# Kernel optimization log

Measured on AMD Instinct MI355X. Metric: run time of the kernel, lower is better.

Reference implementation:

```python
import jax, jax.numpy as jnp
import numpy as np

TOPK = 2
DN = ('NCHW', 'OIHW', 'NCHW')

def gelu(x):
    return jax.nn.gelu(x, approximate=False)

def conv2d(x, w, b, stride, padding, groups):
    y = jax.lax.conv_general_dilated(x, w, stride, padding,
                                     dimension_numbers=DN, feature_group_count=groups)
    return y if b is None else y + b[None, :, None, None]

def setup_inputs() -> dict:
    key = jax.random.key(0)
    ks = jax.random.split(key, 24)
    C, E, L, B, H, W = 64, 4, 5, 16, 160, 160  # L = max low_dim = num_experts+1 (linear growth i+2)
    s = 0.05
    rn = lambda k, shp: jax.random.normal(k, shp, jnp.float32) * s
    d = {}
    d['x'] = jax.random.normal(ks[0], (B, C, H, W), jnp.float32)
    d['c1_w1'] = rn(ks[1], (C, C, 3, 3)); d['c1_b1'] = rn(ks[2], (C,))
    d['c1_w2'] = rn(ks[3], (2 * C, C, 1, 1)); d['c1_b2'] = rn(ks[4], (2 * C,))
    d['agg_w'] = rn(ks[5], (C, 1, 4, 4)); d['agg_b'] = rn(ks[6], (C,))
    d['cal_dw_w'] = rn(ks[7], (C, 1, 3, 3)); d['cal_dw_b'] = rn(ks[8], (C,))
    d['cal_pw_w'] = rn(ks[9], (C, C, 1, 1)); d['cal_pw_b'] = rn(ks[10], (C,))
    d['sc_w1'] = rn(ks[11], (C, 1, 1, 3)); d['sc_b1'] = rn(ks[12], (C,))
    d['sc_w2'] = rn(ks[13], (C, 1, 3, 1)); d['sc_b2'] = rn(ks[14], (C,))
    d['gate_w'] = rn(ks[15], (E, C))
    # Experts have varying low_dim (i+2); zero-pad to L so they stack. Padded
    # channels are exactly zero through the conv1*conv2 product, so math matches.
    rng = np.random.default_rng(0)
    ew1 = np.zeros((E, L, C), np.float32); eb1 = np.zeros((E, L), np.float32)
    ew2 = np.zeros((E, L, C), np.float32); eb2 = np.zeros((E, L), np.float32)
    ew3 = np.zeros((E, C, L), np.float32); eb3 = np.zeros((E, C), np.float32)
    for i in range(E):
        low = i + 2
        ew1[i, :low] = rng.normal(size=(low, C)) * s; eb1[i, :low] = rng.normal(size=(low,)) * s
        ew2[i, :low] = rng.normal(size=(low, C)) * s; eb2[i, :low] = rng.normal(size=(low,)) * s
        ew3[i, :, :low] = rng.normal(size=(C, low)) * s; eb3[i] = rng.normal(size=(C,)) * s
    d['e_w1'] = jnp.asarray(ew1); d['e_b1'] = jnp.asarray(eb1)
    d['e_w2'] = jnp.asarray(ew2); d['e_b2'] = jnp.asarray(eb2)
    d['e_w3'] = jnp.asarray(ew3); d['e_b3'] = jnp.asarray(eb3)
    d['proj_w'] = rn(ks[16], (C, C, 1, 1)); d['proj_b'] = rn(ks[17], (C,))
    return d

def reference(x, c1_w1, c1_b1, c1_w2, c1_b2, agg_w, agg_b, cal_dw_w, cal_dw_b,
              cal_pw_w, cal_pw_b, sc_w1, sc_b1, sc_w2, sc_b2, gate_w,
              e_w1, e_b1, e_w2, e_b2, e_w3, e_b3, proj_w, proj_b):
    B, C = x.shape[0], x.shape[1]
    P1 = [(1, 1), (1, 1)]; P0 = [(0, 0), (0, 0)]
    # conv_1: 3x3 -> GELU -> 1x1 (C -> 2C)
    h = gelu(conv2d(x, c1_w1, c1_b1, (1, 1), P1, 1))
    h = conv2d(h, c1_w2, c1_b2, (1, 1), P0, 1)
    # channel shuffle, groups=2
    b_, c2, hh, ww = h.shape
    h = h.reshape(b_, 2, c2 // 2, hh, ww).transpose(0, 2, 1, 3, 4).reshape(b_, c2, hh, ww)
    xs, k = h[:, :C], h[:, C:]
    # conv_2: striped depthwise (1,3) then (3,1), then GELU
    xs = conv2d(xs, sc_w1, sc_b1, (1, 1), [(0, 0), (1, 1)], C)
    xs = gelu(conv2d(xs, sc_w2, sc_b2, (1, 1), [(1, 1), (0, 0)], C))
    # calibrate(k): recursive depthwise stride-4 downsample, conv, bilinear upsample, residual
    res = k
    for _ in range(2):
        k = gelu(conv2d(k, agg_w, agg_b, (4, 4), [(2, 2), (2, 2)], C))
    k = conv2d(k, cal_dw_w, cal_dw_b, (1, 1), P1, C)
    k = conv2d(k, cal_pw_w, cal_pw_b, (1, 1), P0, 1)
    k = res + jax.image.resize(k, res.shape, method='bilinear')
    # router: global avg pool -> linear (no bias) -> softmax (fp32)
    logits = jnp.mean(xs, axis=(2, 3)) @ gate_w.T  # [B, E]
    weights = jax.nn.softmax(logits.astype(jnp.float32), axis=1).astype(xs.dtype)
    vals, idx = jax.lax.top_k(weights, TOPK)
    exp_w = jnp.zeros_like(weights).at[jnp.arange(B)[:, None], idx].set(vals)  # masked top-k weights
    # dense experts (training path): out = xs + sum_e w_be * Expert_e(xs, k)
    a = jnp.einsum('elc,bchw->belhw', e_w1, xs) + e_b1[None, :, :, None, None]
    bb = jnp.einsum('elc,bchw->belhw', e_w2, k) + e_b2[None, :, :, None, None]
    p = a * bb  # [B, E, L, H, W]
    out = xs + jnp.einsum('be,ecl,belhw->bchw', exp_w, e_w3, p) \
             + jnp.einsum('be,ec->bc', exp_w, e_b3)[:, :, None, None]
    return conv2d(out, proj_w, proj_b, (1, 1), P0, 1)
```

## Files before the change

### kernel.cpp

```cpp
#include <hip/hip_runtime.h>
#include <hip/hip_bf16.h>
#include <math.h>
#include <stdint.h>

typedef __hip_bfloat16 bf16;

__device__ __forceinline__ float b2f(bf16 v){ return __bfloat162float(v); }
__device__ __forceinline__ bf16  f2b(float v){ return __float2bfloat16(v); }
__device__ __forceinline__ float gelu_f(float x){ return 0.5f*x*(1.0f+erff(x*0.70710678118654752f)); }
__device__ __forceinline__ float tof(float v){ return v; }
__device__ __forceinline__ float tof(bf16 v){ return __bfloat162float(v); }

#define SC8  16.0f
#define ISC8 0.0625f
__device__ __forceinline__ uint8_t f2e4(float v){
  int r = __builtin_amdgcn_cvt_pk_fp8_f32(v*SC8, v*SC8, 0, false);
  return (uint8_t)(r & 0xFF);
}
__device__ __forceinline__ float e42f(uint8_t b){
  return __builtin_amdgcn_cvt_f32_fp8((int)b, 0) * ISC8;
}

typedef __bf16 bf16x8 __attribute__((ext_vector_type(8)));
typedef float  f32x4  __attribute__((ext_vector_type(4)));
typedef short  v8s    __attribute__((ext_vector_type(8)));
union Frag { bf16x8 v; unsigned short u[8]; };

__device__ __forceinline__ unsigned short bfb(float v){
  union { bf16 h; unsigned short u; } cv; cv.h = f2b(v); return cv.u;
}
__device__ __forceinline__ float bfu2f(unsigned short u){
  union { float f; unsigned u32; } x; x.u32 = ((unsigned)u) << 16; return x.f;
}
__device__ __forceinline__ bf16x8 ldsb8(const short* p){
  return *reinterpret_cast<const bf16x8*>(p);
}
__device__ __forceinline__ int SW8(int w){ return ((w ^ (w >> 3)) & 7) << 3; }


__global__ __launch_bounds__(256) void k_tr(const float* __restrict__ x,
                                            bf16* __restrict__ xT){
  __shared__ __align__(16) short LT[160*64];
  int bid = blockIdx.x;
  int h = bid % 160;
  int b = bid / 160;
  int tid = threadIdx.x;
  #pragma unroll
  for (int i=0;i<5;i++){
    int q = tid + i*256;
    int ci0 = (q/40)*2;
    int w4  = (q - (q/40)*40)*4;
    const float* pa = x + (((b*64 + ci0)*160 + h)*160) + w4;
    float4 fa = *reinterpret_cast<const float4*>(pa);
    float4 fb = *reinterpret_cast<const float4*>(pa + 25600);
    float va[4] = {fa.x, fa.y, fa.z, fa.w};
    float vb[4] = {fb.x, fb.y, fb.z, fb.w};
    #pragma unroll
    for (int j=0;j<4;j++){
      int w = w4 + j;
      unsigned pk = (unsigned)bfb(va[j]) | ((unsigned)bfb(vb[j]) << 16);
      int slot = w*64 + (ci0 ^ SW8(w));
      *reinterpret_cast<unsigned*>(&LT[slot]) = pk;
    }
  }
  __syncthreads();
  bf16* dst = xT + ((size_t)(b*160 + h))*160*64;
  #pragma unroll
  for (int i=0;i<5;i++){
    int k = tid + i*256;
    int w = k >> 3;
    int ci0 = (k & 7) << 3;
    v8s v = *reinterpret_cast<const v8s*>(&LT[w*64 + (ci0 ^ SW8(w))]);
    *reinterpret_cast<v8s*>(dst + w*64 + ci0) = v;
  }
}

__global__ __launch_bounds__(256) void k_conv12(const bf16* __restrict__ xT,
                                                const float* __restrict__ w1,
                                                const float* __restrict__ b1,
                                                const float* __restrict__ w2,
                                                const float* __restrict__ b2,
                                                bf16* __restrict__ xs0,
                                                bf16* __restrict__ k0){
  __shared__ __align__(16) short Xs[16128];
  __shared__ __align__(16) short H1[5120];
  int bid = blockIdx.x;
  int half = bid & 1;
  int bh = bid >> 1;
  int h = bh % 160;
  int b = bh / 160;
  int w0 = half*80;
  int tid = threadIdx.x;
  int lane = tid & 63;
  int wv = tid >> 6;
  int c = lane & 15;
  int g = lane >> 4;

  Frag wf[18];
  {
    int co = wv*16 + c;
    const float* wbase = w1 + co*576 + g*72;
    #pragma unroll
    for (int r=0;r<3;r++){
      #pragma unroll
      for (int s=0;s<3;s++){
        #pragma unroll
        for (int kk=0;kk<2;kk++){
          Frag f;
          #pragma unroll
          for (int e=0;e<8;e++)
            f.u[e] = bfb(wbase[kk*288 + e*9 + r*3 + s]);
          wf[(r*3+s)*2+kk] = f;
        }
      }
    }
  }

  {
    const bf16* xTb = xT + (size_t)b*160*160*64;
    #pragma unroll
    for (int it=0; it<8; ++it){
      int q = tid + it*256;
      if (q < 2016){
        int r   = q / 672;
        int rem = q - r*672;
        int col = rem >> 3;
        int ci0 = (rem & 7) << 3;
        int gh  = h - 1 + r;
        int gw  = w0 - 1 + col;
        v8s val = {0,0,0,0,0,0,0,0};
        if ((unsigned)gh < 160u && (unsigned)gw < 160u)
          val = *reinterpret_cast<const v8s*>(xTb + (gh*160 + gw)*64 + ci0);
        int eidx = (r*84 + col)*64 + (ci0 ^ ((col & 7) << 3));
        *reinterpret_cast<v8s*>(&Xs[eidx]) = val;
      }
    }
  }
  __syncthreads();

  float bb1r[4];
  {
    const float* bp = b1 + wv*16 + g*4;
    #pragma unroll
    for (int r=0;r<4;r++) bb1r[r] = bp[r];
  }
  int bB[3][2];
  #pragma unroll
  for (int s=0;s<3;s++){
    #pragma unroll
    for (int kk=0;kk<2;kk++)
      bB[s][kk] = (c + s)*64 + ((kk*32 + g*8) ^ (((c + s) & 7) << 3));
  }
  #pragma unroll 1
  for (int n=0;n<5;++n){
    f32x4 acc0 = {0.f,0.f,0.f,0.f};
    f32x4 acc1 = {0.f,0.f,0.f,0.f};
    #pragma unroll
    for (int r=0;r<3;r++){
      #pragma unroll
      for (int s=0;s<3;s++){
        int base = r*5376 + n*1024;
        bf16x8 bf0 = ldsb8(&Xs[bB[s][0] + base]);
        bf16x8 bf1 = ldsb8(&Xs[bB[s][1] + base]);
        int t = (r*3 + s)*2;
        acc0 = __builtin_amdgcn_mfma_f32_16x16x32_bf16(wf[t].v,   bf0, acc0, 0, 0, 0);
        acc1 = __builtin_amdgcn_mfma_f32_16x16x32_bf16(wf[t+1].v, bf1, acc1, 0, 0, 0);
      }
    }
    unsigned long long pk = 0ull;
    #pragma unroll
    for (int r=0;r<4;r++){
      float v = gelu_f(acc0[r] + acc1[r] + bb1r[r]);
      pk |= ((unsigned long long)bfb(v)) << (16*r);
    }
    int eH = (n*16 + c)*64 + ((wv*16 + g*4) ^ ((c & 7) << 3));
    *reinterpret_cast<unsigned long long*>(&H1[eH]) = pk;
  }
  __syncthreads();

  Frag w2f[4];
  {
    #pragma unroll
    for (int j=0;j<2;j++){
      #pragma unroll
      for (int kk=0;kk<2;kk++){
        const float* wp = w2 + (wv*32 + j*16 + c)*64 + kk*32 + g*8;
        Frag f;
        #pragma unroll
        for (int e=0;e<8;e++) f.u[e] = bfb(wp[e]);
        w2f[j*2+kk] = f;
      }
    }
  }
  float bb2r[2][4];
  #pragma unroll
  for (int j=0;j<2;j++){
    const float* bp = b2 + wv*32 + j*16 + g*4;
    #pragma unroll
    for (int r=0;r<4;r++) bb2r[j][r] = bp[r];
  }
  int posb = h*160 + w0 + c;
  int sb[2][4]; int flg[2][4];
  #pragma unroll
  for (int j=0;j<2;j++){
    #pragma unroll
    for (int r=0;r<4;r++){
      int o = wv*32 + j*16 + g*4 + r;
      int n2 = ((o & 63) << 1) | (o >> 6);
      if (n2 < 64){ sb[j][r] = (b*64 + n2)*25600 + posb;        flg[j][r] = 1; }
      else        { sb[j][r] = (b*64 + (n2-64))*25600 + posb;   flg[j][r] = 0; }
    }
  }
  int bH0 = c*64 + ((g*8)      ^ ((c & 7) << 3));
  int bH1 = c*64 + ((32 + g*8) ^ ((c & 7) << 3));
  #pragma unroll 1
  for (int n=0;n<5;++n){
    bf16x8 h0 = ldsb8(&H1[bH0 + n*1024]);
    bf16x8 h1 = ldsb8(&H1[bH1 + n*1024]);
    #pragma unroll
    for (int j=0;j<2;j++){
      f32x4 acc = {0.f,0.f,0.f,0.f};
      acc = __builtin_amdgcn_mfma_f32_16x16x32_bf16(w2f[j*2].v,   h0, acc, 0, 0, 0);
      acc = __builtin_amdgcn_mfma_f32_16x16x32_bf16(w2f[j*2+1].v, h1, acc, 0, 0, 0);
      #pragma unroll
      for (int r=0;r<4;r++){
        float v = acc[r] + bb2r[j][r];
        bf16 bv = f2b(v);
        if (flg[j][r]) xs0[sb[j][r] + n*16] = bv;
        else           k0 [sb[j][r] + n*16] = bv;
      }
    }
  }
}

__global__ __launch_bounds__(256) void k_sc(const bf16* __restrict__ xs0,
                                            const float* __restrict__ scw1,
                                            const float* __restrict__ scb1,
                                            const float* __restrict__ scw2,
                                            const float* __restrict__ scb2,
                                            bf16* __restrict__ xsf){
  int t = blockIdx.x*256 + threadIdx.x;
  int w8 = (t % 20) * 8;
  int r2 = t / 20;
  int h  = r2 % 160;
  int bc = r2 / 160;
  int c  = bc & 63;
  const bf16* plane = xs0 + (size_t)bc*25600;
  float w1a = scw1[c*3], w1b = scw1[c*3+1], w1c = scw1[c*3+2];
  float b1  = scb1[c];
  float w2a = scw2[c*3], w2b = scw2[c*3+1], w2c = scw2[c*3+2];
  float b2v = scb2[c];
  float acc[8];
  #pragma unroll
  for (int j=0;j<8;j++) acc[j] = b2v;
  #pragma unroll
  for (int dh=0; dh<3; dh++){
    int hh = h-1+dh;
    if ((unsigned)hh < 160u){
      const bf16* row = plane + hh*160;
      float wnd[10];
      v8s mv = *reinterpret_cast<const v8s*>(row + w8);
      #pragma unroll
      for (int j=0;j<8;j++) wnd[j+1] = bfu2f((unsigned short)mv[j]);
      wnd[0] = (w8 > 0)   ? b2f(row[w8-1]) : 0.f;
      wnd[9] = (w8 < 152) ? b2f(row[w8+8]) : 0.f;
      float w2h = (dh==0)?w2a:((dh==1)?w2b:w2c);
      #pragma unroll
      for (int j=0;j<8;j++){
        float inner = fmaf(w1a, wnd[j], fmaf(w1b, wnd[j+1], fmaf(w1c, wnd[j+2], b1)));
        acc[j] = fmaf(w2h, inner, acc[j]);
      }
    }
  }
  v8s o;
  #pragma unroll
  for (int j=0;j<8;j++) o[j] = (short)bfb(gelu_f(acc[j]));
  *reinterpret_cast<v8s*>(xsf + (size_t)bc*25600 + h*160 + w8) = o;
}

__global__ __launch_bounds__(256) void k_mean(const bf16* __restrict__ xsf, float* __restrict__ meanX){
  int bc = blockIdx.x;
  const bf16* p = xsf + (size_t)bc*25600;
  float s = 0.f;
  for (int i = threadIdx.x; i < 3200; i += 256){
    v8s v = *reinterpret_cast<const v8s*>(p + i*8);
    #pragma unroll
    for (int j=0;j<8;j++) s += bfu2f((unsigned short)v[j]);
  }
  __shared__ float red[256];
  red[threadIdx.x] = s; __syncthreads();
  for (int st=128; st>0; st>>=1){
    if (threadIdx.x < st) red[threadIdx.x] += red[threadIdx.x+st];
    __syncthreads();
  }
  if (threadIdx.x==0) meanX[bc] = red[0]*(1.0f/25600.0f);
}

template<typename Tin>
__global__ __launch_bounds__(256) void k_agg(const Tin* __restrict__ in,
                                             const float* __restrict__ aggw,
                                             const float* __restrict__ aggb,
                                             float* __restrict__ out,
                                             int IH, int OH, int total){
  int t = blockIdx.x*256+threadIdx.x;
  if (t >= total) return;
  int ow = t % OH;
  int oh = (t/OH) % OH;
  int c  = (t/(OH*OH)) & 63;
  int bc = t/(OH*OH);
  const Tin* ip = in + (size_t)bc*IH*IH;
  const float* Wp = aggw + c*16;
  float acc = aggb[c];
  #pragma unroll
  for (int kh=0;kh<4;kh++){
    int ih = oh*4 - 2 + kh;
    if ((unsigned)ih < (unsigned)IH){
      #pragma unroll
      for (int kw=0;kw<4;kw++){
        int iw = ow*4 - 2 + kw;
        if ((unsigned)iw < (unsigned)IH)
          acc = fmaf(Wp[kh*4+kw], tof(ip[ih*IH+iw]), acc);
      }
    }
  }
  out[t] = gelu_f(acc);
}

__global__ __launch_bounds__(256) void k_caldw(const float* __restrict__ A2,
                                               const float* __restrict__ dww,
                                               const float* __restrict__ dwb,
                                               float* __restrict__ T1){
  int t = blockIdx.x*256+threadIdx.x;
  if (t >= 16*64*121) return;
  int pw = t % 11;
  int ph = (t/11) % 11;
  int c  = (t/121) & 63;
  int bc = t/121;
  const float* ip = A2 + bc*121;
  const float* Wp = dww + c*9;
  float acc = dwb[c];
  #pragma unroll
  for (int kh=0;kh<3;kh++){
    int ih = ph-1+kh;
    if ((unsigned)ih < 11u){
      #pragma unroll
      for (int kw=0;kw<3;kw++){
        int iw = pw-1+kw;
        if ((unsigned)iw < 11u)
          acc = fmaf(Wp[kh*3+kw], ip[ih*11+iw], acc);
      }
    }
  }
  T1[t] = acc;
}

__global__ __launch_bounds__(256) void k_calpw(const float* __restrict__ T1,
                                               const float* __restrict__ pww,
                                               const float* __restrict__ pwb,
                                               float* __restrict__ KSo){
  int t = blockIdx.x*256+threadIdx.x;
  if (t >= 16*64*121) return;
  int p  = t % 121;
  int co = (t/121) & 63;
  int b  = t/(121*64);
  const float* Wp = pww + co*64;
  const float* ip = T1 + b*64*121 + p;
  float acc = pwb[co];
  for (int ci=0;ci<64;ci++) acc = fmaf(Wp[ci], ip[ci*121], acc);
  KSo[t] = acc;
}

__global__ __launch_bounds__(64) void k_gate(const float* __restrict__ meanX,
                                             const float* __restrict__ gatew,
                                             float* __restrict__ expw){
  __shared__ float lg[64];
  int t = threadIdx.x;
  int b = t>>2, e = t&3;
  const float* g = gatew + e*64;
  const float* m = meanX + b*64;
  float s = 0.f;
  for (int c2=0;c2<64;c2++) s += g[c2]*m[c2];
  lg[t] = s;
  __syncthreads();
  if (e==0){
    float v0=lg[t], v1=lg[t+1], v2=lg[t+2], v3=lg[t+3];
    float mx = fmaxf(fmaxf(v0,v1), fmaxf(v2,v3));
    float p[4];
    p[0]=expf(v0-mx); p[1]=expf(v1-mx); p[2]=expf(v2-mx); p[3]=expf(v3-mx);
    float sum = p[0]+p[1]+p[2]+p[3];
    float inv = 1.0f/sum;
    p[0]*=inv; p[1]*=inv; p[2]*=inv; p[3]*=inv;
    int i1 = 0;
    for (int i=1;i<4;i++) if (p[i] > p[i1]) i1 = i;
    int i2 = -1;
    for (int i=0;i<4;i++){ if (i==i1) continue; if (i2<0 || p[i]>p[i2]) i2 = i; }
    for (int i=0;i<4;i++) expw[b*4+i] = (i==i1||i==i2)? p[i] : 0.f;
  }
}

__global__ __launch_bounds__(256) void k_pw3(const float* __restrict__ ew3,
                                             const float* __restrict__ eb3,
                                             const float* __restrict__ projw,
                                             float* __restrict__ pw3,
                                             float* __restrict__ pb3){
  int t = blockIdx.x*256+threadIdx.x;
  if (t >= 64*24) return;
  int r = t/24, q = t%24;
  const float* P = projw + r*64;
  if (q < 20){
    int e=q/5, l=q%5;
    float s=0.f;
    for (int c=0;c<64;c++) s = fmaf(P[c], ew3[(e*64+c)*5 + l], s);
    pw3[r*20+q] = s;
  } else {
    int e = q-20;
    float s=0.f;
    for (int c=0;c<64;c++) s = fmaf(P[c], eb3[e*64 + c], s);
    pb3[r*4+e] = s;
  }
}

__global__ __launch_bounds__(256) void k_kk(const bf16* __restrict__ k0,
                                            const float* __restrict__ KSi,
                                            uint8_t* __restrict__ kk8){
  int tt = blockIdx.x*256 + threadIdx.x;
  int bc = tt / 3200;
  int rr = tt - bc*3200;
  int ph = rr / 20;
  int pw0 = (rr - ph*20) * 8;
  float shf = (ph+0.5f)*0.06875f - 0.5f;
  int ihf = (int)floorf(shf); float th = shf - (float)ihf;
  int i0 = min(max(ihf,0),10), i1 = min(max(ihf+1,0),10);
  const float* ksp = KSi + bc*121;
  size_t base = (size_t)bc*25600 + ph*160 + pw0;
  v8s kv = *reinterpret_cast<const v8s*>(k0 + base);
  unsigned long long o = 0ull;
  #pragma unroll
  for (int j=0;j<8;j++){
    int pw = pw0 + j;
    float swf = (pw+0.5f)*0.06875f - 0.5f;
    int iwf = (int)floorf(swf); float tw = swf - (float)iwf;
    int j0 = min(max(iwf,0),10), j1 = min(max(iwf+1,0),10);
    float v00 = ksp[i0*11+j0], v01 = ksp[i0*11+j1];
    float v10 = ksp[i1*11+j0], v11 = ksp[i1*11+j1];
    float vtop = v00 + tw*(v01-v00);
    float vbot = v10 + tw*(v11-v10);
    float val = bfu2f((unsigned short)kv[j]) + (vtop + th*(vbot-vtop));
    o |= ((unsigned long long)f2e4(val)) << (8*j);
  }
  *reinterpret_cast<unsigned long long*>(kk8 + base) = o;
}

__global__ __launch_bounds__(256) void k_final(const bf16* __restrict__ xsf,
                                               const uint8_t* __restrict__ kk8,
                                               const float* __restrict__ expw,
                                               const float* __restrict__ pw3,
                                               const float* __restrict__ pb3,
                                               const float* __restrict__ ew1,
                                               const float* __restrict__ eb1,
                                               const float* __restrict__ ew2,
                                               const float* __restrict__ eb2,
                                               const float* __restrict__ projw,
                                               const float* __restrict__ projb,
                                               float* __restrict__ out){
  __shared__ float XS[4096];
  __shared__ float KK[4096];
  __shared__ float PP[1280];
  int bid = blockIdx.x;
  int pt = bid % 400;
  int b  = bid / 400;
  int p0 = pt<<6;
  int tid = threadIdx.x;
  int lane = tid & 63;
  for (int cw = tid; cw < 512; cw += 256){
    int c = cw >> 3, w0 = (cw & 7) << 3;
    size_t gi = (size_t)(b*64+c)*25600 + p0 + w0;
    v8s xv = *reinterpret_cast<const v8s*>(xsf + gi);
    unsigned long long kv = *reinterpret_cast<const unsigned long long*>(kk8 + gi);
    #pragma unroll
    for (int j=0;j<8;j++){
      XS[(c<<6)+w0+j] = bfu2f((unsigned short)xv[j]);
      KK[(c<<6)+w0+j] = e42f((uint8_t)((kv >> (8*j)) & 0xFF));
    }
  }
  __syncthreads();
  int wv = __builtin_amdgcn_readfirstlane(tid>>6);
  {
    int e = wv;
    float a[5], bb[5];
    #pragma unroll
    for (int l=0;l<5;l++) a[l] = eb1[e*5 + l];
    const float* W1 = ew1 + e*5*64;
    for (int c=0;c<64;c++){
      float xv = XS[(c<<6)+lane];
      #pragma unroll
      for (int l=0;l<5;l++) a[l] = fmaf(W1[l*64+c], xv, a[l]);
    }
    #pragma unroll
    for (int l=0;l<5;l++) bb[l] = eb2[e*5 + l];
    const float* W2 = ew2 + e*5*64;
    for (int c=0;c<64;c++){
      float kv = KK[(c<<6)+lane];
      #pragma unroll
      for (int l=0;l<5;l++) bb[l] = fmaf(W2[l*64+c], kv, bb[l]);
    }
    float we = expw[b*4 + e];
    #pragma unroll
    for (int l=0;l<5;l++) PP[(e*5+l)*64 + lane] = we * a[l]*bb[l];
  }
  __syncthreads();
  float ew0 = expw[b*4+0], ewa = expw[b*4+1], ewb = expw[b*4+2], ewc = expw[b*4+3];
  for (int qg=0; qg<4; qg++){
    int r0 = (wv<<4) + (qg<<2);
    float y[4];
    #pragma unroll
    for (int q=0;q<4;q++){
      int r = r0+q;
      y[q] = projb[r] + ew0*pb3[r*4+0] + ewa*pb3[r*4+1] + ewb*pb3[r*4+2] + ewc*pb3[r*4+3];
    }
    const float* Pw = projw + r0*64;
    for (int c=0;c<64;c++){
      float xv = XS[(c<<6)+lane];
      y[0]=fmaf(Pw[c]     ,xv,y[0]);
      y[1]=fmaf(Pw[64+c]  ,xv,y[1]);
      y[2]=fmaf(Pw[128+c] ,xv,y[2]);
      y[3]=fmaf(Pw[192+c] ,xv,y[3]);
    }
    const float* Qw = pw3 + r0*20;
    for (int j=0;j<20;j++){
      float pv = PP[(j<<6)+lane];
      y[0]=fmaf(Qw[j]    ,pv,y[0]);
      y[1]=fmaf(Qw[20+j] ,pv,y[1]);
      y[2]=fmaf(Qw[40+j] ,pv,y[2]);
      y[3]=fmaf(Qw[60+j] ,pv,y[3]);
    }
    #pragma unroll
    for (int q=0;q<4;q++)
      out[(size_t)(b*64+r0+q)*25600 + p0 + lane] = y[q];
  }
}

static constexpr size_t OB_XT   = 0;
static constexpr size_t OB_K0   = 52428800;
static constexpr size_t OB_MEAN = 0;
static constexpr size_t OB_KS   = 65536;
static constexpr size_t OB_A2   = 1048576;
static constexpr size_t OB_T1   = 2097152;
static constexpr size_t OB_A1   = 4194304;
static constexpr size_t XB_XS0  = 0;
static constexpr size_t XB_KK8  = 0;
static constexpr size_t XB_EXPW = 26214400;
static constexpr size_t XB_PW3  = 26218496;
static constexpr size_t XB_PB3  = 26226688;
static constexpr size_t XB_XSF  = 52428800;

extern "C" void kernel_launch(void* const* d_in, const int* in_sizes, int n_in,
                              void* d_out, int out_size, void* d_ws, size_t ws_size,
                              hipStream_t stream){
  (void)in_sizes; (void)n_in; (void)out_size; (void)d_ws; (void)ws_size;
  const float* x     = (const float*)d_in[0];
  char* xb           = (char*)d_in[0];
  const float* c1w1  = (const float*)d_in[1];
  const float* c1b1  = (const float*)d_in[2];
  const float* c1w2  = (const float*)d_in[3];
  const float* c1b2  = (const float*)d_in[4];
  const float* aggw  = (const float*)d_in[5];
  const float* aggb  = (const float*)d_in[6];
  const float* dww   = (const float*)d_in[7];
  const float* dwb   = (const float*)d_in[8];
  const float* pww   = (const float*)d_in[9];
  const float* pwb   = (const float*)d_in[10];
  const float* scw1  = (const float*)d_in[11];
  const float* scb1  = (const float*)d_in[12];
  const float* scw2  = (const float*)d_in[13];
  const float* scb2  = (const float*)d_in[14];
  const float* gatew = (const float*)d_in[15];
  const float* ew1   = (const float*)d_in[16];
  const float* eb1   = (const float*)d_in[17];
  const float* ew2   = (const float*)d_in[18];
  const float* eb2   = (const float*)d_in[19];
  const float* ew3   = (const float*)d_in[20];
  const float* eb3   = (const float*)d_in[21];
  const float* projw = (const float*)d_in[22];
  const float* projb = (const float*)d_in[23];

  char* ob = (char*)d_out;
  bf16* xT     = (bf16*)(ob + OB_XT);
  bf16* k0     = (bf16*)(ob + OB_K0);
  float* meanX = (float*)(ob + OB_MEAN);
  float* KS    = (float*)(ob + OB_KS);
  float* A2    = (float*)(ob + OB_A2);
  float* T1    = (float*)(ob + OB_T1);
  float* A1    = (float*)(ob + OB_A1);
  bf16* xs0    = (bf16*)(xb + XB_XS0);
  uint8_t* kk8 = (uint8_t*)(xb + XB_KK8);
  float* expw  = (float*)(xb + XB_EXPW);
  float* pw3   = (float*)(xb + XB_PW3);
  float* pb3   = (float*)(xb + XB_PB3);
  bf16* xsf    = (bf16*)(xb + XB_XSF);
  float* outp  = (float*)d_out;

  k_tr     <<<2560,     256, 0, stream>>>(x, xT);
  k_conv12 <<<5120,     256, 0, stream>>>(xT, c1w1, c1b1, c1w2, c1b2, xs0, k0);
  k_sc     <<<12800,    256, 0, stream>>>(xs0, scw1, scb1, scw2, scb2, xsf);
  k_mean   <<<1024,     256, 0, stream>>>(xsf, meanX);
  k_agg<bf16> <<<6724,  256, 0, stream>>>(k0, aggw, aggb, A1, 160, 41, 16*64*41*41);
  k_agg<float><<<484,   256, 0, stream>>>(A1, aggw, aggb, A2, 41, 11, 16*64*11*11);
  k_caldw  <<<484,      256, 0, stream>>>(A2, dww, dwb, T1);
  k_calpw  <<<484,      256, 0, stream>>>(T1, pww, pwb, KS);
  k_gate   <<<1,         64, 0, stream>>>(meanX, gatew, expw);
  k_pw3    <<<6,        256, 0, stream>>>(ew3, eb3, projw, pw3, pb3);
  k_kk     <<<12800,    256, 0, stream>>>(k0, KS, kk8);
  k_final  <<<16*400,   256, 0, stream>>>(xsf, kk8, expw, pw3, pb3,
                                          ew1, eb1, ew2, eb2, projw, projb, outp);
}
```

Baseline: 621.6 us.

## Fuse mean into shortcut kernel and fuse aggregation chain into one kernel

The global-average-pool mean is now computed inside the shortcut-conv kernel with a wavefront shuffle reduction and atomicAdd, after zeroing the buffer in a small kernel. This removes the separate full re-read of xsf. The two stride-4 aggregation convs and the depthwise calibration conv are fused into one kernel per (b,c) plane that stages the plane in LDS and keeps the intermediates in shared memory, which removes the global A1/A2 round-trips and two launches. In exchange, atomics make the summation order nondeterministic. The large LDS footprint of about 58KB per block limits occupancy of the fused kernel to 1024 blocks.

```diff
diff --git a/kernel.cpp b/kernel.cpp
--- a/kernel.cpp
+++ b/kernel.cpp
@@ -8,8 +8,6 @@
 __device__ __forceinline__ float b2f(bf16 v){ return __bfloat162float(v); }
 __device__ __forceinline__ bf16  f2b(float v){ return __float2bfloat16(v); }
 __device__ __forceinline__ float gelu_f(float x){ return 0.5f*x*(1.0f+erff(x*0.70710678118654752f)); }
-__device__ __forceinline__ float tof(float v){ return v; }
-__device__ __forceinline__ float tof(bf16 v){ return __bfloat162float(v); }
 
 #define SC8  16.0f
 #define ISC8 0.0625f
@@ -73,6 +71,10 @@
     v8s v = *reinterpret_cast<const v8s*>(&LT[w*64 + (ci0 ^ SW8(w))]);
     *reinterpret_cast<v8s*>(dst + w*64 + ci0) = v;
   }
+}
+
+__global__ __launch_bounds__(256) void k_zero(float* __restrict__ p){
+  p[blockIdx.x*256 + threadIdx.x] = 0.f;
 }
 
 __global__ __launch_bounds__(256) void k_conv12(const bf16* __restrict__ xT,
@@ -238,7 +240,8 @@
                                             const float* __restrict__ scb1,
                                             const float* __restrict__ scw2,
                                             const float* __restrict__ scb2,
-                                            bf16* __restrict__ xsf){
+                                            bf16* __restrict__ xsf,
+                                            float* __restrict__ meanX){
   int t = blockIdx.x*256 + threadIdx.x;
   int w8 = (t % 20) * 8;
   int r2 = t / 20;
@@ -273,85 +276,92 @@
     }
   }
   v8s o;
-  #pragma unroll
-  for (int j=0;j<8;j++) o[j] = (short)bfb(gelu_f(acc[j]));
+  float ls = 0.f;
+  #pragma unroll
+  for (int j=0;j<8;j++){
+    unsigned short ub = bfb(gelu_f(acc[j]));
+    o[j] = (short)ub;
+    ls += bfu2f(ub);
+  }
   *reinterpret_cast<v8s*>(xsf + (size_t)bc*25600 + h*160 + w8) = o;
-}
-
-__global__ __launch_bounds__(256) void k_mean(const bf16* __restrict__ xsf, float* __restrict__ meanX){
+  #pragma unroll
+  for (int off=32; off>0; off>>=1) ls += __shfl_down(ls, off);
+  if ((threadIdx.x & 63) == 0) atomicAdd(&meanX[bc], ls*(1.0f/25600.0f));
+}
+
+__global__ __launch_bounds__(256) void k_aggfuse(const bf16* __restrict__ k0,
+                                                 const float* __restrict__ aggw,
+                                                 const float* __restrict__ aggb,
+                                                 const float* __restrict__ dww,
+                                                 const float* __restrict__ dwb,
+                                                 float* __restrict__ T1){
+  __shared__ __align__(16) short KP[25600];
+  __shared__ float A1L[1681];
+  __shared__ float A2L[121];
   int bc = blockIdx.x;
-  const bf16* p = xsf + (size_t)bc*25600;
-  float s = 0.f;
-  for (int i = threadIdx.x; i < 3200; i += 256){
-    v8s v = *reinterpret_cast<const v8s*>(p + i*8);
-    #pragma unroll
-    for (int j=0;j<8;j++) s += bfu2f((unsigned short)v[j]);
-  }
-  __shared__ float red[256];
-  red[threadIdx.x] = s; __syncthreads();
-  for (int st=128; st>0; st>>=1){
-    if (threadIdx.x < st) red[threadIdx.x] += red[threadIdx.x+st];
-    __syncthreads();
-  }
-  if (threadIdx.x==0) meanX[bc] = red[0]*(1.0f/25600.0f);
-}
-
-template<typename Tin>
-__global__ __launch_bounds__(256) void k_agg(const Tin* __restrict__ in,
-                                             const float* __restrict__ aggw,
-                                             const float* __restrict__ aggb,
-                                             float* __restrict__ out,
-                                             int IH, int OH, int total){
-  int t = blockIdx.x*256+threadIdx.x;
-  if (t >= total) return;
-  int ow = t % OH;
-  int oh = (t/OH) % OH;
-  int c  = (t/(OH*OH)) & 63;
-  int bc = t/(OH*OH);
-  const Tin* ip = in + (size_t)bc*IH*IH;
-  const float* Wp = aggw + c*16;
-  float acc = aggb[c];
-  #pragma unroll
-  for (int kh=0;kh<4;kh++){
-    int ih = oh*4 - 2 + kh;
-    if ((unsigned)ih < (unsigned)IH){
-      #pragma unroll
-      for (int kw=0;kw<4;kw++){
-        int iw = ow*4 - 2 + kw;
-        if ((unsigned)iw < (unsigned)IH)
-          acc = fmaf(Wp[kh*4+kw], tof(ip[ih*IH+iw]), acc);
-      }
-    }
-  }
-  out[t] = gelu_f(acc);
-}
-
-__global__ __launch_bounds__(256) void k_caldw(const float* __restrict__ A2,
-                                               const float* __restrict__ dww,
-                                               const float* __restrict__ dwb,
-                                               float* __restrict__ T1){
-  int t = blockIdx.x*256+threadIdx.x;
-  if (t >= 16*64*121) return;
-  int pw = t % 11;
-  int ph = (t/11) % 11;
-  int c  = (t/121) & 63;
-  int bc = t/121;
-  const float* ip = A2 + bc*121;
-  const float* Wp = dww + c*9;
-  float acc = dwb[c];
-  #pragma unroll
-  for (int kh=0;kh<3;kh++){
-    int ih = ph-1+kh;
-    if ((unsigned)ih < 11u){
-      #pragma unroll
-      for (int kw=0;kw<3;kw++){
-        int iw = pw-1+kw;
-        if ((unsigned)iw < 11u)
-          acc = fmaf(Wp[kh*3+kw], ip[ih*11+iw], acc);
-      }
-    }
-  }
-  T1[t] = acc;
+  int c = bc & 63;
+  int tid = threadIdx.x;
+  const bf16* src = k0 + (size_t)bc*25600;
+  for (int i=tid; i<3200; i+=256)
+    *reinterpret_cast<v8s*>(&KP[i*8]) = *reinterpret_cast<const v8s*>(src + i*8);
+  float wgt[16];
+  #pragma unroll
+  for (int q=0;q<16;q++) wgt[q] = aggw[c*16+q];
+  float bia = aggb[c];
+  __syncthreads();
+  for (int i=tid; i<1681; i+=256){
+    int oh = i/41, ow = i - oh*41;
+    float acc = bia;
+    #pragma unroll
+    for (int kh=0;kh<4;kh++){
+      int ih = oh*4-2+kh;
+      if ((unsigned)ih < 160u){
+        #pragma unroll
+        for (int kw=0;kw<4;kw++){
+          int iw = ow*4-2+kw;
+          if ((unsigned)iw < 160u)
+            acc = fmaf(wgt[kh*4+kw], bfu2f((unsigned short)KP[ih*160+iw]), acc);
+        }
+      }
+    }
+    A1L[i] = gelu_f(acc);
+  }
+  __syncthreads();
+  if (tid < 121){
+    int ph = tid/11, pw = tid - ph*11;
+    float acc = bia;
+    #pragma unroll
+    for (int kh=0;kh<4;kh++){
+      int ih = ph*4-2+kh;
+      if ((unsigned)ih < 41u){
+        #pragma unroll
+        for (int kw=0;kw<4;kw++){
+          int iw = pw*4-2+kw;
+          if ((unsigned)iw < 41u)
+            acc = fmaf(wgt[kh*4+kw], A1L[ih*41+iw], acc);
+        }
+      }
+    }
+    A2L[tid] = gelu_f(acc);
+  }
+  __syncthreads();
+  if (tid < 121){
+    int ph = tid/11, pw = tid - ph*11;
+    float acc = dwb[c];
+    #pragma unroll
+    for (int kh=0;kh<3;kh++){
+      int ih = ph-1+kh;
+      if ((unsigned)ih < 11u){
+        #pragma unroll
+        for (int kw=0;kw<3;kw++){
+          int iw = pw-1+kw;
+          if ((unsigned)iw < 11u)
+            acc = fmaf(dww[c*9+kh*3+kw], A2L[ih*11+iw], acc);
+        }
+      }
+    }
+    T1[(size_t)bc*121 + tid] = acc;
+  }
 }
 
 __global__ __launch_bounds__(256) void k_calpw(const float* __restrict__ T1,
@@ -544,9 +554,7 @@
 static constexpr size_t OB_K0   = 52428800;
 static constexpr size_t OB_MEAN = 0;
 static constexpr size_t OB_KS   = 65536;
-static constexpr size_t OB_A2   = 1048576;
 static constexpr size_t OB_T1   = 2097152;
-static constexpr size_t OB_A1   = 4194304;
 static constexpr size_t XB_XS0  = 0;
 static constexpr size_t XB_KK8  = 0;
 static constexpr size_t XB_EXPW = 26214400;
@@ -589,9 +597,7 @@
   bf16* k0     = (bf16*)(ob + OB_K0);
   float* meanX = (float*)(ob + OB_MEAN);
   float* KS    = (float*)(ob + OB_KS);
-  float* A2    = (float*)(ob + OB_A2);
   float* T1    = (float*)(ob + OB_T1);
-  float* A1    = (float*)(ob + OB_A1);
   bf16* xs0    = (bf16*)(xb + XB_XS0);
   uint8_t* kk8 = (uint8_t*)(xb + XB_KK8);
   float* expw  = (float*)(xb + XB_EXPW);
@@ -602,11 +608,9 @@
 
   k_tr     <<<2560,     256, 0, stream>>>(x, xT);
   k_conv12 <<<5120,     256, 0, stream>>>(xT, c1w1, c1b1, c1w2, c1b2, xs0, k0);
-  k_sc     <<<12800,    256, 0, stream>>>(xs0, scw1, scb1, scw2, scb2, xsf);
-  k_mean   <<<1024,     256, 0, stream>>>(xsf, meanX);
-  k_agg<bf16> <<<6724,  256, 0, stream>>>(k0, aggw, aggb, A1, 160, 41, 16*64*41*41);
-  k_agg<float><<<484,   256, 0, stream>>>(A1, aggw, aggb, A2, 41, 11, 16*64*11*11);
-  k_caldw  <<<484,      256, 0, stream>>>(A2, dww, dwb, T1);
+  k_zero   <<<4,        256, 0, stream>>>(meanX);
+  k_sc     <<<12800,    256, 0, stream>>>(xs0, scw1, scb1, scw2, scb2, xsf, meanX);
+  k_aggfuse<<<1024,     256, 0, stream>>>(k0, aggw, aggb, dww, dwb, T1);
   k_calpw  <<<484,      256, 0, stream>>>(T1, pww, pwb, KS);
   k_gate   <<<1,         64, 0, stream>>>(meanX, gatew, expw);
   k_pw3    <<<6,        256, 0, stream>>>(ew3, eb3, projw, pw3, pb3);
```

Result: slower. 647.2 us (+4.1%).

## Process 5-row strips in conv12 with rolling halo buffer; fuse mean into sc

Applied to the files above, without the earlier changes.

Each conv12 block now handles a strip of 5 output rows instead of one row. It keeps a 4-slot ring buffer of input rows in LDS and prefetches the next row into registers while the current row's MFMAs run. This cuts the 3x halo reload of input rows and amortizes the per-block weight fragment loads over more rows. Separately, the global-mean kernel is removed: k_sc accumulates per-wavefront partial sums into meanX with atomics after a small zeroing kernel. The trade-offs are fewer blocks (1024), extra per-row syncs, and float atomic nondeterminism in the mean.

```diff
diff --git a/kernel.cpp b/kernel.cpp
--- a/kernel.cpp
+++ b/kernel.cpp
@@ -75,6 +75,10 @@
   }
 }
 
+__global__ __launch_bounds__(256) void k_zero(float* __restrict__ p){
+  p[blockIdx.x*256 + threadIdx.x] = 0.f;
+}
+
 __global__ __launch_bounds__(256) void k_conv12(const bf16* __restrict__ xT,
                                                 const float* __restrict__ w1,
                                                 const float* __restrict__ b1,
@@ -82,19 +86,20 @@
                                                 const float* __restrict__ b2,
                                                 bf16* __restrict__ xs0,
                                                 bf16* __restrict__ k0){
-  __shared__ __align__(16) short Xs[16128];
+  __shared__ __align__(16) short Xs[4*5376];
   __shared__ __align__(16) short H1[5120];
   int bid = blockIdx.x;
-  int half = bid & 1;
-  int bh = bid >> 1;
-  int h = bh % 160;
-  int b = bh / 160;
-  int w0 = half*80;
+  int strip = bid & 31;
+  int half  = (bid >> 5) & 1;
+  int b     = bid >> 6;
+  int h0 = strip * 5;
+  int w0 = half * 80;
   int tid = threadIdx.x;
   int lane = tid & 63;
   int wv = tid >> 6;
   int c = lane & 15;
   int g = lane >> 4;
+  const bf16* xTb = xT + (size_t)b*160*160*64;
 
   Frag wf[18];
   {
@@ -115,69 +120,6 @@
       }
     }
   }
-
-  {
-    const bf16* xTb = xT + (size_t)b*160*160*64;
-    #pragma unroll
-    for (int it=0; it<8; ++it){
-      int q = tid + it*256;
-      if (q < 2016){
-        int r   = q / 672;
-        int rem = q - r*672;
-        int col = rem >> 3;
-        int ci0 = (rem & 7) << 3;
-        int gh  = h - 1 + r;
-        int gw  = w0 - 1 + col;
-        v8s val = {0,0,0,0,0,0,0,0};
-        if ((unsigned)gh < 160u && (unsigned)gw < 160u)
-          val = *reinterpret_cast<const v8s*>(xTb + (gh*160 + gw)*64 + ci0);
-        int eidx = (r*84 + col)*64 + (ci0 ^ ((col & 7) << 3));
-        *reinterpret_cast<v8s*>(&Xs[eidx]) = val;
-      }
-    }
-  }
-  __syncthreads();
-
-  float bb1r[4];
-  {
-    const float* bp = b1 + wv*16 + g*4;
-    #pragma unroll
-    for (int r=0;r<4;r++) bb1r[r] = bp[r];
-  }
-  int bB[3][2];
-  #pragma unroll
-  for (int s=0;s<3;s++){
-    #pragma unroll
-    for (int kk=0;kk<2;kk++)
-      bB[s][kk] = (c + s)*64 + ((kk*32 + g*8) ^ (((c + s) & 7) << 3));
-  }
-  #pragma unroll 1
-  for (int n=0;n<5;++n){
-    f32x4 acc0 = {0.f,0.f,0.f,0.f};
-    f32x4 acc1 = {0.f,0.f,0.f,0.f};
-    #pragma unroll
-    for (int r=0;r<3;r++){
-      #pragma unroll
-      for (int s=0;s<3;s++){
-        int base = r*5376 + n*1024;
-        bf16x8 bf0 = ldsb8(&Xs[bB[s][0] + base]);
-        bf16x8 bf1 = ldsb8(&Xs[bB[s][1] + base]);
-        int t = (r*3 + s)*2;
-        acc0 = __builtin_amdgcn_mfma_f32_16x16x32_bf16(wf[t].v,   bf0, acc0, 0, 0, 0);
-        acc1 = __builtin_amdgcn_mfma_f32_16x16x32_bf16(wf[t+1].v, bf1, acc1, 0, 0, 0);
-      }
-    }
-    unsigned long long pk = 0ull;
-    #pragma unroll
-    for (int r=0;r<4;r++){
-      float v = gelu_f(acc0[r] + acc1[r] + bb1r[r]);
-      pk |= ((unsigned long long)bfb(v)) << (16*r);
-    }
-    int eH = (n*16 + c)*64 + ((wv*16 + g*4) ^ ((c & 7) << 3));
-    *reinterpret_cast<unsigned long long*>(&H1[eH]) = pk;
-  }
-  __syncthreads();
-
   Frag w2f[4];
   {
     #pragma unroll
@@ -192,6 +134,12 @@
       }
     }
   }
+  float bb1r[4];
+  {
+    const float* bp = b1 + wv*16 + g*4;
+    #pragma unroll
+    for (int r=0;r<4;r++) bb1r[r] = bp[r];
+  }
   float bb2r[2][4];
   #pragma unroll
   for (int j=0;j<2;j++){
@@ -199,37 +147,126 @@
     #pragma unroll
     for (int r=0;r<4;r++) bb2r[j][r] = bp[r];
   }
-  int posb = h*160 + w0 + c;
-  int sb[2][4]; int flg[2][4];
+  int cb[2][4]; int flg[2][4];
   #pragma unroll
   for (int j=0;j<2;j++){
     #pragma unroll
     for (int r=0;r<4;r++){
       int o = wv*32 + j*16 + g*4 + r;
       int n2 = ((o & 63) << 1) | (o >> 6);
-      if (n2 < 64){ sb[j][r] = (b*64 + n2)*25600 + posb;        flg[j][r] = 1; }
-      else        { sb[j][r] = (b*64 + (n2-64))*25600 + posb;   flg[j][r] = 0; }
-    }
+      if (n2 < 64){ cb[j][r] = (b*64 + n2)*25600 + w0 + c;        flg[j][r] = 1; }
+      else        { cb[j][r] = (b*64 + (n2-64))*25600 + w0 + c;   flg[j][r] = 0; }
+    }
+  }
+  int bB[3][2];
+  #pragma unroll
+  for (int s=0;s<3;s++){
+    #pragma unroll
+    for (int kk=0;kk<2;kk++)
+      bB[s][kk] = (c + s)*64 + ((kk*32 + g*8) ^ (((c + s) & 7) << 3));
   }
   int bH0 = c*64 + ((g*8)      ^ ((c & 7) << 3));
   int bH1 = c*64 + ((32 + g*8) ^ ((c & 7) << 3));
+
+  #pragma unroll
+  for (int it=0; it<8; ++it){
+    int q = tid + it*256;
+    if (q < 2016){
+      int r   = q / 672;
+      int rem = q - r*672;
+      int col = rem >> 3;
+      int ci0 = (rem & 7) << 3;
+      int gh  = h0 - 1 + r;
+      int gw  = w0 - 1 + col;
+      v8s val = {0,0,0,0,0,0,0,0};
+      if ((unsigned)gh < 160u && (unsigned)gw < 160u)
+        val = *reinterpret_cast<const v8s*>(xTb + (gh*160 + gw)*64 + ci0);
+      int slot = (gh + 1) & 3;
+      *reinterpret_cast<v8s*>(&Xs[slot*5376 + col*64 + (ci0 ^ ((col & 7) << 3))]) = val;
+    }
+  }
+  __syncthreads();
+
   #pragma unroll 1
-  for (int n=0;n<5;++n){
-    bf16x8 h0 = ldsb8(&H1[bH0 + n*1024]);
-    bf16x8 h1 = ldsb8(&H1[bH1 + n*1024]);
-    #pragma unroll
-    for (int j=0;j<2;j++){
-      f32x4 acc = {0.f,0.f,0.f,0.f};
-      acc = __builtin_amdgcn_mfma_f32_16x16x32_bf16(w2f[j*2].v,   h0, acc, 0, 0, 0);
-      acc = __builtin_amdgcn_mfma_f32_16x16x32_bf16(w2f[j*2+1].v, h1, acc, 0, 0, 0);
+  for (int row=0; row<5; ++row){
+    int h = h0 + row;
+    v8s stv[3]; int stq[3];
+    #pragma unroll
+    for (int it=0; it<3; ++it){
+      int q = tid + it*256;
+      stq[it] = (q < 672 && row < 4) ? q : -1;
+      v8s val = {0,0,0,0,0,0,0,0};
+      if (stq[it] >= 0){
+        int col = q >> 3;
+        int ci0 = (q & 7) << 3;
+        int gh  = h + 2;
+        int gw  = w0 - 1 + col;
+        if (gh < 160 && (unsigned)gw < 160u)
+          val = *reinterpret_cast<const v8s*>(xTb + (gh*160 + gw)*64 + ci0);
+      }
+      stv[it] = val;
+    }
+    int sb0 = ((h  ) & 3) * 5376;
+    int sb1 = ((h+1) & 3) * 5376;
+    int sb2 = ((h+2) & 3) * 5376;
+    #pragma unroll 1
+    for (int n=0;n<5;++n){
+      f32x4 acc0 = {0.f,0.f,0.f,0.f};
+      f32x4 acc1 = {0.f,0.f,0.f,0.f};
+      #pragma unroll
+      for (int r=0;r<3;r++){
+        int base = (r==0?sb0:(r==1?sb1:sb2)) + n*1024;
+        #pragma unroll
+        for (int s=0;s<3;s++){
+          bf16x8 bf0 = ldsb8(&Xs[bB[s][0] + base]);
+          bf16x8 bf1 = ldsb8(&Xs[bB[s][1] + base]);
+          int t = (r*3 + s)*2;
+          acc0 = __builtin_amdgcn_mfma_f32_16x16x32_bf16(wf[t].v,   bf0, acc0, 0, 0, 0);
+          acc1 = __builtin_amdgcn_mfma_f32_16x16x32_bf16(wf[t+1].v, bf1, acc1, 0, 0, 0);
+        }
+      }
+      unsigned long long pk = 0ull;
       #pragma unroll
       for (int r=0;r<4;r++){
-        float v = acc[r] + bb2r[j][r];
-        bf16 bv = f2b(v);
-        if (flg[j][r]) xs0[sb[j][r] + n*16] = bv;
-        else           k0 [sb[j][r] + n*16] = bv;
-      }
-    }
+        float v = gelu_f(acc0[r] + acc1[r] + bb1r[r]);
+        pk |= ((unsigned long long)bfb(v)) << (16*r);
+      }
+      int eH = (n*16 + c)*64 + ((wv*16 + g*4) ^ ((c & 7) << 3));
+      *reinterpret_cast<unsigned long long*>(&H1[eH]) = pk;
+    }
+    {
+      int slot = (h + 3) & 3;
+      #pragma unroll
+      for (int it=0; it<3; ++it){
+        if (stq[it] >= 0){
+          int col = stq[it] >> 3;
+          int ci0 = (stq[it] & 7) << 3;
+          *reinterpret_cast<v8s*>(&Xs[slot*5376 + col*64 + (ci0 ^ ((col & 7) << 3))]) = stv[it];
+        }
+      }
+    }
+    __syncthreads();
+    int posb = h*160;
+    #pragma unroll 1
+    for (int n=0;n<5;++n){
+      bf16x8 hh0 = ldsb8(&H1[bH0 + n*1024]);
+      bf16x8 hh1 = ldsb8(&H1[bH1 + n*1024]);
+      #pragma unroll
+      for (int j=0;j<2;j++){
+        f32x4 acc = {0.f,0.f,0.f,0.f};
+        acc = __builtin_amdgcn_mfma_f32_16x16x32_bf16(w2f[j*2].v,   hh0, acc, 0, 0, 0);
+        acc = __builtin_amdgcn_mfma_f32_16x16x32_bf16(w2f[j*2+1].v, hh1, acc, 0, 0, 0);
+        #pragma unroll
+        for (int r=0;r<4;r++){
+          float v = acc[r] + bb2r[j][r];
+          bf16 bv = f2b(v);
+          int addr = cb[j][r] + posb + n*16;
+          if (flg[j][r]) xs0[addr] = bv;
+          else           k0 [addr] = bv;
+        }
+      }
+    }
+    __syncthreads();
   }
 }
 
@@ -238,7 +275,8 @@
                                             const float* __restrict__ scb1,
                                             const float* __restrict__ scw2,
                                             const float* __restrict__ scb2,
-                                            bf16* __restrict__ xsf){
+                                            bf16* __restrict__ xsf,
+                                            float* __restrict__ meanX){
   int t = blockIdx.x*256 + threadIdx.x;
   int w8 = (t % 20) * 8;
   int r2 = t / 20;
@@ -273,27 +311,17 @@
     }
   }
   v8s o;
-  #pragma unroll
-  for (int j=0;j<8;j++) o[j] = (short)bfb(gelu_f(acc[j]));
+  float ls = 0.f;
+  #pragma unroll
+  for (int j=0;j<8;j++){
+    unsigned short ub = bfb(gelu_f(acc[j]));
+    o[j] = (short)ub;
+    ls += bfu2f(ub);
+  }
   *reinterpret_cast<v8s*>(xsf + (size_t)bc*25600 + h*160 + w8) = o;
-}
-
-__global__ __launch_bounds__(256) void k_mean(const bf16* __restrict__ xsf, float* __restrict__ meanX){
-  int bc = blockIdx.x;
-  const bf16* p = xsf + (size_t)bc*25600;
-  float s = 0.f;
-  for (int i = threadIdx.x; i < 3200; i += 256){
-    v8s v = *reinterpret_cast<const v8s*>(p + i*8);
-    #pragma unroll
-    for (int j=0;j<8;j++) s += bfu2f((unsigned short)v[j]);
-  }
-  __shared__ float red[256];
-  red[threadIdx.x] = s; __syncthreads();
-  for (int st=128; st>0; st>>=1){
-    if (threadIdx.x < st) red[threadIdx.x] += red[threadIdx.x+st];
-    __syncthreads();
-  }
-  if (threadIdx.x==0) meanX[bc] = red[0]*(1.0f/25600.0f);
+  #pragma unroll
+  for (int off=32; off>0; off>>=1) ls += __shfl_down(ls, off);
+  if ((threadIdx.x & 63) == 0) atomicAdd(&meanX[bc], ls*(1.0f/25600.0f));
 }
 
 template<typename Tin>
@@ -601,9 +629,9 @@
   float* outp  = (float*)d_out;
 
   k_tr     <<<2560,     256, 0, stream>>>(x, xT);
-  k_conv12 <<<5120,     256, 0, stream>>>(xT, c1w1, c1b1, c1w2, c1b2, xs0, k0);
-  k_sc     <<<12800,    256, 0, stream>>>(xs0, scw1, scb1, scw2, scb2, xsf);
-  k_mean   <<<1024,     256, 0, stream>>>(xsf, meanX);
+  k_conv12 <<<1024,     256, 0, stream>>>(xT, c1w1, c1b1, c1w2, c1b2, xs0, k0);
+  k_zero   <<<4,        256, 0, stream>>>(meanX);
+  k_sc     <<<12800,    256, 0, stream>>>(xs0, scw1, scb1, scw2, scb2, xsf, meanX);
   k_agg<bf16> <<<6724,  256, 0, stream>>>(k0, aggw, aggb, A1, 160, 41, 16*64*41*41);
   k_agg<float><<<484,   256, 0, stream>>>(A1, aggw, aggb, A2, 41, 11, 16*64*11*11);
   k_caldw  <<<484,      256, 0, stream>>>(A2, dww, dwb, T1);
```

Result: faster. 576.8 us (-7.2%).
